# Performance work log

Measured on AMD Instinct MI355X. Metric: run time of the kernel, lower is better.

Reference implementation:

```python
import jax, jax.numpy as jnp
import numpy as np

D_MODEL = 4096
NUM_EXPERTS = 64
TOP_K = 2


def setup_inputs() -> dict:
    key = jax.random.key(0)
    kx, kw, kb = jax.random.split(key, 3)
    x = jax.random.normal(kx, (4, 4096, D_MODEL), dtype=jnp.float32)
    # nn.Linear(d_model, num_experts): weight [E, D], bias [E]
    bound = 1.0 / np.sqrt(D_MODEL)
    W = jax.random.uniform(kw, (NUM_EXPERTS, D_MODEL), jnp.float32, -bound, bound)
    b = jax.random.uniform(kb, (NUM_EXPERTS,), jnp.float32, -bound, bound)
    return {"x": x, "W": W, "b": b}


def reference(x, W, b):
    # gate: logits over experts  [B, S, E]
    logits = jnp.einsum("bsd,ed->bse", x, W) + b
    # top-k experts per token
    top_w, top_i = jax.lax.top_k(logits, TOP_K)  # [B, S, K]
    # softmax over the selected k logits
    top_w = jax.nn.softmax(top_w, axis=-1)
    return top_w, top_i
```

## Files before the change

kernel.cpp:

```cpp
#include <hip/hip_runtime.h>
#include <math.h>

#define D_MODEL 4096
#define NE 64
#define TPB 64
#define NSTEPS 32
#define XBUF 32768
#define NXBUF 4
#define WS_SHORTS (256 * 2 * 64 * 8)

typedef __attribute__((ext_vector_type(8))) short short8;
typedef __attribute__((ext_vector_type(16))) float f32x16;

__device__ __forceinline__ void gl_lds(const void* g, void* l) {
    __builtin_amdgcn_global_load_lds(
        (const __attribute__((address_space(1))) unsigned*)g,
        (__attribute__((address_space(3))) unsigned*)l, 16, 0, 0);
}

__device__ __forceinline__ void split8(const float4& a, const float4& c,
                                       short8& h8, short8& l8) {
    union { short8 s; unsigned u[4]; } H, L;
    float vv[8] = {a.x, a.y, a.z, a.w, c.x, c.y, c.z, c.w};
#pragma unroll
    for (int p = 0; p < 4; p++) {
        const float v0 = vv[2*p], v1 = vv[2*p+1];
        const unsigned u0 = __float_as_uint(v0), u1 = __float_as_uint(v1);
        const unsigned r0 = u0 + 0x7fffu + ((u0 >> 16) & 1u);
        const unsigned r1 = u1 + 0x7fffu + ((u1 >> 16) & 1u);
        const float lo0 = v0 - __uint_as_float(r0 & 0xffff0000u);
        const float lo1 = v1 - __uint_as_float(r1 & 0xffff0000u);
        H.u[p] = __builtin_amdgcn_perm(r1, r0, 0x07060302u);
        L.u[p] = __builtin_amdgcn_perm(__float_as_uint(lo1),
                                       __float_as_uint(lo0), 0x07060302u);
    }
    h8 = H.s; l8 = L.s;
}

__global__ void wsplit_kernel(const float* __restrict__ W, short* __restrict__ wsp) {
    const int ck = blockIdx.x, t = threadIdx.x;
    const int nt = t >> 6, l = t & 63;
    const float* wp = W + (size_t)(nt * 32 + (l & 31)) * D_MODEL + ck * 16 + (l >> 5) * 8;
    float4 a = *(const float4*)wp, c = *(const float4*)(wp + 4);
    union { short8 s; unsigned u[4]; } H, L;
    float vv[8] = {a.x, a.y, a.z, a.w, c.x, c.y, c.z, c.w};
#pragma unroll
    for (int p = 0; p < 4; p++) {
        const float v0 = vv[2*p], v1 = vv[2*p+1];
        const unsigned u0 = __float_as_uint(v0), u1 = __float_as_uint(v1);
        const unsigned r0 = u0 + 0x7fffu + ((u0 >> 16) & 1u);
        const unsigned r1 = u1 + 0x7fffu + ((u1 >> 16) & 1u);
        const float lo0 = v0 - __uint_as_float(r0 & 0xffff0000u);
        const float lo1 = v1 - __uint_as_float(r1 & 0xffff0000u);
        const unsigned q0 = __float_as_uint(lo0) + 0x7fffu + ((__float_as_uint(lo0) >> 16) & 1u);
        const unsigned q1 = __float_as_uint(lo1) + 0x7fffu + ((__float_as_uint(lo1) >> 16) & 1u);
        H.u[p] = __builtin_amdgcn_perm(r1, r0, 0x07060302u);
        L.u[p] = __builtin_amdgcn_perm(q1, q0, 0x07060302u);
    }
    const size_t off = ((size_t)(ck * 2 + nt) * 64 + l) * 8;
    *(short8*)(wsp + off)             = H.s;
    *(short8*)(wsp + WS_SHORTS + off) = L.s;
}

#define MF(A_, B_, n_) acc[n_] = __builtin_amdgcn_mfma_f32_32x32x16_bf16( \
                             A_, B_, acc[n_], 0, 0, 0)

__global__ __launch_bounds__(512, 2) void router_pipe(
    const float* __restrict__ x, const short* __restrict__ wsp,
    const float* __restrict__ b, float* __restrict__ out, int T)
{
    __shared__ char smem[NXBUF * XBUF];

    const int tid  = threadIdx.x;
    const int wv   = tid >> 6, lane = tid & 63;
    const int mt   = wv & 1;
    const int kq   = wv >> 1;
    const int tok0 = blockIdx.x * TPB;

    const int tokA = tid >> 4, clA = tid & 15;
    const int tokB = 32 + tokA;
    const float* gx1 = x + (size_t)(tok0 + tokA) * D_MODEL + ((clA ^ (tokA & 15)) * 4);
    const float* gx2 = x + (size_t)(tok0 + tokB) * D_MODEL + ((clA ^ (tokB & 15)) * 4);

#define STAGEX(s_, bi_) do { char* db_ = smem + (bi_) * XBUF + wv * 1024;      \
        gl_lds(gx1 + (size_t)(s_) * 128,      db_);                            \
        gl_lds(gx2 + (size_t)(s_) * 128,      db_ + 8192);                     \
        gl_lds(gx1 + (size_t)(s_) * 128 + 64, db_ + 16384);                    \
        gl_lds(gx2 + (size_t)(s_) * 128 + 64, db_ + 24576);                    \
        __builtin_amdgcn_sched_barrier(0); } while (0)

#define LDW(s_, W0_,W1_,W2_,W3_,W4_,W5_,W6_,W7_) do {                          \
        const size_t cg0_ = (size_t)(s_) * 8 + kq * 2;                         \
        const size_t a0_ = ((cg0_ * 2 + 0) * 64 + lane) * 8;                   \
        const size_t a1_ = ((cg0_ * 2 + 1) * 64 + lane) * 8;                   \
        const size_t a2_ = (((cg0_ + 1) * 2 + 0) * 64 + lane) * 8;             \
        const size_t a3_ = (((cg0_ + 1) * 2 + 1) * 64 + lane) * 8;             \
        W0_ = *(const short8*)(wsp + a0_);                                     \
        W1_ = *(const short8*)(wsp + a1_);                                     \
        W2_ = *(const short8*)(wsp + WS_SHORTS + a0_);                         \
        W3_ = *(const short8*)(wsp + WS_SHORTS + a1_);                         \
        W4_ = *(const short8*)(wsp + a2_);                                     \
        W5_ = *(const short8*)(wsp + a3_);                                     \
        W6_ = *(const short8*)(wsp + WS_SHORTS + a2_);                         \
        W7_ = *(const short8*)(wsp + WS_SHORTS + a3_);                         \
        __builtin_amdgcn_sched_barrier(0); } while (0)

#define FENCE(n_) do { asm volatile("s_waitcnt vmcnt(" #n_ ")" ::: "memory");  \
        __builtin_amdgcn_sched_barrier(0); } while (0)
#define BAR do { __builtin_amdgcn_s_barrier();                                 \
        __builtin_amdgcn_sched_barrier(0); } while (0)

    f32x16 acc[2];
#pragma unroll
    for (int e = 0; e < 16; e++) { acc[0][e] = 0.f; acc[1][e] = 0.f; }

    const int row = mt * 32 + (lane & 31);
    const int cA  = kq * 8 + (lane >> 5) * 2;
#define XOFF(c_) (((c_) >> 4) * 16384 + row * 256 + ((((c_) & 15) ^ (row & 15)) * 16))
    const int xoA0 = XOFF(cA),     xoA1 = XOFF(cA + 1);
    const int xoB0 = XOFF(cA + 4), xoB1 = XOFF(cA + 5);

#define COMPUTE(bi_, W0_,W1_,W2_,W3_,W4_,W5_,W6_,W7_) do {                     \
        const char* buf_ = smem + (bi_) * XBUF;                                \
        { float4 xa_ = *(const float4*)(buf_ + xoA0);                          \
          float4 xb_ = *(const float4*)(buf_ + xoA1);                          \
          short8 Ah_, Al_; split8(xa_, xb_, Ah_, Al_);                         \
          MF(Ah_, W0_, 0); MF(Ah_, W2_, 0); MF(Al_, W0_, 0); MF(Al_, W2_, 0);  \
          MF(Ah_, W1_, 1); MF(Ah_, W3_, 1); MF(Al_, W1_, 1); MF(Al_, W3_, 1); }\
        { float4 xa_ = *(const float4*)(buf_ + xoB0);                          \
          float4 xb_ = *(const float4*)(buf_ + xoB1);                          \
          short8 Ah_, Al_; split8(xa_, xb_, Ah_, Al_);                         \
          MF(Ah_, W4_, 0); MF(Ah_, W6_, 0); MF(Al_, W4_, 0); MF(Al_, W6_, 0);  \
          MF(Ah_, W5_, 1); MF(Ah_, W7_, 1); MF(Al_, W5_, 1); MF(Al_, W7_, 1); }\
        } while (0)

    short8 Wa0, Wa1, Wa2, Wa3, Wa4, Wa5, Wa6, Wa7;
    short8 Wb0, Wb1, Wb2, Wb3, Wb4, Wb5, Wb6, Wb7;

    STAGEX(0, 0); STAGEX(1, 1);
    LDW(0, Wa0,Wa1,Wa2,Wa3,Wa4,Wa5,Wa6,Wa7);

    for (int t = 0; t < NSTEPS - 2; t += 2) {
        LDW(t + 1, Wb0,Wb1,Wb2,Wb3,Wb4,Wb5,Wb6,Wb7);
        STAGEX(t + 2, (t + 2) & 3);
        FENCE(16); BAR;
        COMPUTE(t & 3, Wa0,Wa1,Wa2,Wa3,Wa4,Wa5,Wa6,Wa7);
        LDW(t + 2, Wa0,Wa1,Wa2,Wa3,Wa4,Wa5,Wa6,Wa7);
        STAGEX(t + 3, (t + 3) & 3);
        FENCE(16); BAR;
        COMPUTE((t + 1) & 3, Wb0,Wb1,Wb2,Wb3,Wb4,Wb5,Wb6,Wb7);
    }
    LDW(NSTEPS - 1, Wb0,Wb1,Wb2,Wb3,Wb4,Wb5,Wb6,Wb7);
    FENCE(12); BAR;
    COMPUTE((NSTEPS - 2) & 3, Wa0,Wa1,Wa2,Wa3,Wa4,Wa5,Wa6,Wa7);
    FENCE(0); BAR;
    COMPUTE((NSTEPS - 1) & 3, Wb0,Wb1,Wb2,Wb3,Wb4,Wb5,Wb6,Wb7);

    __syncthreads();

    float* red = (float*)smem;
    auto store_slab = [&](int slab) {
        float* sl = red + ((size_t)slab * 64 + lane) * 32;
#pragma unroll
        for (int q = 0; q < 8; q++) {
            const int nt = q >> 2, rg = (q & 3) * 4;
            *(float4*)(sl + ((q + lane) & 7) * 4) =
                make_float4(acc[nt][rg], acc[nt][rg+1], acc[nt][rg+2], acc[nt][rg+3]);
        }
    };
    auto add_slab = [&](int slab) {
        const float* sl = red + ((size_t)slab * 64 + lane) * 32;
#pragma unroll
        for (int q = 0; q < 8; q++) {
            const int nt = q >> 2, rg = (q & 3) * 4;
            float4 v = *(const float4*)(sl + ((q + lane) & 7) * 4);
            acc[nt][rg] += v.x; acc[nt][rg+1] += v.y;
            acc[nt][rg+2] += v.z; acc[nt][rg+3] += v.w;
        }
    };
    if (kq >= 2) store_slab(mt * 2 + (kq - 2));
    __syncthreads();
    if (kq < 2) add_slab(mt * 2 + kq);
    __syncthreads();
    if (kq == 1) store_slab(mt);
    __syncthreads();
    if (kq == 0) add_slab(mt);
    __syncthreads();

    float* lg = (float*)(smem + 32768);
    if (kq == 0) {
        const int h = lane >> 5, c31 = lane & 31;
        const float bb0 = b[c31], bb1 = b[32 + c31];
#pragma unroll
        for (int nt = 0; nt < 2; nt++) {
#pragma unroll
            for (int e = 0; e < 16; e++) {
                const int r2 = (e & 3) + 8 * (e >> 2) + 4 * h;
                lg[(mt * 32 + r2) * 68 + nt * 32 + c31] = acc[nt][e] + (nt ? bb1 : bb0);
            }
        }
    }
    __syncthreads();

    if (tid < TPB) {
        const float4* rowp = (const float4*)(lg + tid * 68);
        float v0 = -INFINITY, v1 = -INFINITY;
        int i0 = 0, i1 = 0;
#pragma unroll
        for (int q = 0; q < 16; q++) {
            float4 v4 = rowp[q];
            float vs[4] = {v4.x, v4.y, v4.z, v4.w};
#pragma unroll
            for (int j = 0; j < 4; j++) {
                const int e = q * 4 + j;
                const float v = vs[j];
                if (v > v0)      { v1 = v0; i1 = i0; v0 = v; i0 = e; }
                else if (v > v1) { v1 = v;  i1 = e; }
            }
        }
        const float e1 = expf(v1 - v0);
        const float w0 = 1.f / (1.f + e1);
        const int tok = tok0 + tid;
        out[tok * 2 + 0] = w0;
        out[tok * 2 + 1] = e1 * w0;
        float* oi = out + (size_t)T * 2;
        oi[tok * 2 + 0] = (float)i0;
        oi[tok * 2 + 1] = (float)i1;
    }
}

__global__ __launch_bounds__(512, 4) void router_fb(
    const float* __restrict__ x, const float* __restrict__ W,
    const float* __restrict__ b, float* __restrict__ out, int T)
{
    __shared__ short smem[16384];
    const int tid = threadIdx.x;
    const int wv = tid >> 6, lane = tid & 63;
    const int tok0 = blockIdx.x * 32;
    const int row = lane & 31, kh = lane >> 5;
    const float* gx = x + (size_t)(tok0 + row) * D_MODEL + wv * 512 + kh * 8;
    f32x16 acc[2];
#pragma unroll
    for (int e = 0; e < 16; e++) { acc[0][e] = 0.f; acc[1][e] = 0.f; }
    for (int s = 0; s < 32; s++) {
        const float* g = gx + (size_t)s * 16;
        float4 xa = *(const float4*)g, xb = *(const float4*)(g + 4);
        const int k0 = wv * 512 + s * 16 + kh * 8;
        const float* w0 = W + (size_t)row * D_MODEL + k0;
        const float* w1 = W + (size_t)(32 + row) * D_MODEL + k0;
        short8 Ah, Al, B0h, B0l, B1h, B1l;
        split8(xa, xb, Ah, Al);
        split8(*(const float4*)w0, *(const float4*)(w0 + 4), B0h, B0l);
        split8(*(const float4*)w1, *(const float4*)(w1 + 4), B1h, B1l);
        MF(Ah, B0h, 0); MF(Ah, B0l, 0); MF(Al, B0h, 0); MF(Al, B0l, 0);
        MF(Ah, B1h, 1); MF(Ah, B1l, 1); MF(Al, B1h, 1); MF(Al, B1l, 1);
    }
    float* red = (float*)smem;
    auto store_slab = [&](int slab) {
        float* sl = red + ((size_t)slab * 64 + lane) * 32;
#pragma unroll
        for (int q = 0; q < 8; q++) {
            const int nt = q >> 2, rg = (q & 3) * 4;
            *(float4*)(sl + ((q + lane) & 7) * 4) =
                make_float4(acc[nt][rg], acc[nt][rg+1], acc[nt][rg+2], acc[nt][rg+3]);
        }
    };
    auto add_slab = [&](int slab) {
        const float* sl = red + ((size_t)slab * 64 + lane) * 32;
#pragma unroll
        for (int q = 0; q < 8; q++) {
            const int nt = q >> 2, rg = (q & 3) * 4;
            float4 v = *(const float4*)(sl + ((q + lane) & 7) * 4);
            acc[nt][rg] += v.x; acc[nt][rg+1] += v.y;
            acc[nt][rg+2] += v.z; acc[nt][rg+3] += v.w;
        }
    };
    __syncthreads();
    if (wv >= 4) store_slab(wv - 4);
    __syncthreads();
    if (wv < 4) add_slab(wv);
    __syncthreads();
    if (wv == 2 || wv == 3) store_slab(wv - 2);
    __syncthreads();
    if (wv < 2) add_slab(wv);
    __syncthreads();
    if (wv == 1) store_slab(0);
    __syncthreads();
    if (wv == 0) add_slab(0);
    __syncthreads();
    float* lg = (float*)smem;
    if (wv == 0) {
        const int h = lane >> 5, c31 = lane & 31;
        const float bb0 = b[c31], bb1 = b[32 + c31];
#pragma unroll
        for (int nt = 0; nt < 2; nt++)
#pragma unroll
            for (int e = 0; e < 16; e++) {
                const int r2 = (e & 3) + 8 * (e >> 2) + 4 * h;
                lg[r2 * 68 + nt * 32 + c31] = acc[nt][e] + (nt ? bb1 : bb0);
            }
    }
    __syncthreads();
    if (tid < 32) {
        const float4* rowp = (const float4*)(lg + tid * 68);
        float v0 = -INFINITY, v1 = -INFINITY;
        int i0 = 0, i1 = 0;
#pragma unroll
        for (int q = 0; q < 16; q++) {
            float4 v4 = rowp[q];
            float vs[4] = {v4.x, v4.y, v4.z, v4.w};
#pragma unroll
            for (int j = 0; j < 4; j++) {
                const float v = vs[j];
                if (v > v0)      { v1 = v0; i1 = i0; v0 = v; i0 = q*4+j; }
                else if (v > v1) { v1 = v;  i1 = q*4+j; }
            }
        }
        const float e1 = expf(v1 - v0);
        const float w0 = 1.f / (1.f + e1);
        const int tok = tok0 + tid;
        out[tok * 2 + 0] = w0;
        out[tok * 2 + 1] = e1 * w0;
        float* oi = out + (size_t)T * 2;
        oi[tok * 2 + 0] = (float)i0;
        oi[tok * 2 + 1] = (float)i1;
    }
}

extern "C" void kernel_launch(void* const* d_in, const int* in_sizes, int n_in,
                              void* d_out, int out_size, void* d_ws, size_t ws_size,
                              hipStream_t stream) {
    const float* x = (const float*)d_in[0];
    const float* W = (const float*)d_in[1];
    const float* b = (const float*)d_in[2];
    float* out = (float*)d_out;
    short* wsp = (short*)d_ws;
    const int T = in_sizes[0] / D_MODEL;

    const bool pre = (ws_size >= (size_t)(2 * WS_SHORTS) * sizeof(short));
    if (pre) {
        hipLaunchKernelGGL(wsplit_kernel, dim3(256), dim3(128), 0, stream, W, wsp);
        hipLaunchKernelGGL(router_pipe, dim3(T / TPB), dim3(512), 0, stream,
                           x, wsp, b, out, T);
    } else {
        hipLaunchKernelGGL(router_fb, dim3(T / 32), dim3(512), 0, stream,
                           x, W, b, out, T);
    }
}
```

Measured before the change: 63.86 us.

## Give each wave private LDS staging buffers and drop per-step block barriers

Reorganizes x staging so each wave loads exactly the 32 tokens and K-slice it consumes into its own 16KB LDS region, with a new XOR swizzle. Because no wave reads data written by another wave, the per-step s_barrier is removed and only vmcnt waits remain. This is meant to cut barrier stalls and let waves run out of lockstep. The trade-off is that each x element is now staged redundantly by the waves that need it, and correctness depends on the wave-local vmcnt fence covering the LDS writes from global_load_lds.

```diff
diff --git a/kernel.cpp b/kernel.cpp
--- a/kernel.cpp
+++ b/kernel.cpp
@@ -5,8 +5,6 @@
 #define NE 64
 #define TPB 64
 #define NSTEPS 32
-#define XBUF 32768
-#define NXBUF 4
 #define WS_SHORTS (256 * 2 * 64 * 8)
 
 typedef __attribute__((ext_vector_type(8))) short short8;
@@ -69,7 +67,7 @@
     const float* __restrict__ x, const short* __restrict__ wsp,
     const float* __restrict__ b, float* __restrict__ out, int T)
 {
-    __shared__ char smem[NXBUF * XBUF];
+    __shared__ char smem[131072];
 
     const int tid  = threadIdx.x;
     const int wv   = tid >> 6, lane = tid & 63;
@@ -77,16 +75,18 @@
     const int kq   = wv >> 1;
     const int tok0 = blockIdx.x * TPB;
 
-    const int tokA = tid >> 4, clA = tid & 15;
-    const int tokB = 32 + tokA;
-    const float* gx1 = x + (size_t)(tok0 + tokA) * D_MODEL + ((clA ^ (tokA & 15)) * 4);
-    const float* gx2 = x + (size_t)(tok0 + tokB) * D_MODEL + ((clA ^ (tokB & 15)) * 4);
-
-#define STAGEX(s_, bi_) do { char* db_ = smem + (bi_) * XBUF + wv * 1024;      \
-        gl_lds(gx1 + (size_t)(s_) * 128,      db_);                            \
-        gl_lds(gx2 + (size_t)(s_) * 128,      db_ + 8192);                     \
-        gl_lds(gx1 + (size_t)(s_) * 128 + 64, db_ + 16384);                    \
-        gl_lds(gx2 + (size_t)(s_) * 128 + 64, db_ + 24576);                    \
+    char* const wbuf = smem + wv * 16384;
+
+    const char* gxl = (const char*)x
+        + (size_t)(tok0 + mt * 32 + (lane >> 3)) * 16384
+        + kq * 128 + (((lane & 7) ^ (lane >> 3)) * 16);
+
+#define STAGEX(s_, bi_) do { char* db_ = wbuf + (bi_) * 4096;                  \
+        const char* g_ = gxl + (size_t)(s_) * 512;                             \
+        gl_lds(g_,          db_);                                              \
+        gl_lds(g_ + 131072, db_ + 1024);                                       \
+        gl_lds(g_ + 262144, db_ + 2048);                                       \
+        gl_lds(g_ + 393216, db_ + 3072);                                       \
         __builtin_amdgcn_sched_barrier(0); } while (0)
 
 #define LDW(s_, W0_,W1_,W2_,W3_,W4_,W5_,W6_,W7_) do {                          \
@@ -107,21 +107,19 @@
 
 #define FENCE(n_) do { asm volatile("s_waitcnt vmcnt(" #n_ ")" ::: "memory");  \
         __builtin_amdgcn_sched_barrier(0); } while (0)
-#define BAR do { __builtin_amdgcn_s_barrier();                                 \
-        __builtin_amdgcn_sched_barrier(0); } while (0)
 
     f32x16 acc[2];
 #pragma unroll
     for (int e = 0; e < 16; e++) { acc[0][e] = 0.f; acc[1][e] = 0.f; }
 
-    const int row = mt * 32 + (lane & 31);
-    const int cA  = kq * 8 + (lane >> 5) * 2;
-#define XOFF(c_) (((c_) >> 4) * 16384 + row * 256 + ((((c_) & 15) ^ (row & 15)) * 16))
-    const int xoA0 = XOFF(cA),     xoA1 = XOFF(cA + 1);
-    const int xoB0 = XOFF(cA + 4), xoB1 = XOFF(cA + 5);
+    const int rw = lane & 31, khalf = lane >> 5;
+    const int rbase = (rw >> 3) * 1024 + (rw & 7) * 128;
+#define XO(ck_, j_) (rbase + (((((ck_) * 4) + khalf * 2 + (j_)) ^ (rw & 7)) * 16))
+    const int xoA0 = XO(0, 0), xoA1 = XO(0, 1);
+    const int xoB0 = XO(1, 0), xoB1 = XO(1, 1);
 
 #define COMPUTE(bi_, W0_,W1_,W2_,W3_,W4_,W5_,W6_,W7_) do {                     \
-        const char* buf_ = smem + (bi_) * XBUF;                                \
+        const char* buf_ = wbuf + (bi_) * 4096;                                \
         { float4 xa_ = *(const float4*)(buf_ + xoA0);                          \
           float4 xb_ = *(const float4*)(buf_ + xoA1);                          \
           short8 Ah_, Al_; split8(xa_, xb_, Ah_, Al_);                         \
@@ -143,17 +141,17 @@
     for (int t = 0; t < NSTEPS - 2; t += 2) {
         LDW(t + 1, Wb0,Wb1,Wb2,Wb3,Wb4,Wb5,Wb6,Wb7);
         STAGEX(t + 2, (t + 2) & 3);
-        FENCE(16); BAR;
+        FENCE(16);
         COMPUTE(t & 3, Wa0,Wa1,Wa2,Wa3,Wa4,Wa5,Wa6,Wa7);
         LDW(t + 2, Wa0,Wa1,Wa2,Wa3,Wa4,Wa5,Wa6,Wa7);
         STAGEX(t + 3, (t + 3) & 3);
-        FENCE(16); BAR;
+        FENCE(16);
         COMPUTE((t + 1) & 3, Wb0,Wb1,Wb2,Wb3,Wb4,Wb5,Wb6,Wb7);
     }
     LDW(NSTEPS - 1, Wb0,Wb1,Wb2,Wb3,Wb4,Wb5,Wb6,Wb7);
-    FENCE(12); BAR;
+    FENCE(12);
     COMPUTE((NSTEPS - 2) & 3, Wa0,Wa1,Wa2,Wa3,Wa4,Wa5,Wa6,Wa7);
-    FENCE(0); BAR;
+    FENCE(0);
     COMPUTE((NSTEPS - 1) & 3, Wb0,Wb1,Wb2,Wb3,Wb4,Wb5,Wb6,Wb7);
 
     __syncthreads();
```

Result: slower. 68.14 us (+6.7%).
